# Optimization experiments

Measured on AMD Instinct MI355X. Metric: run time of the kernel, lower is better.

Reference implementation:

```python
import jax, jax.numpy as jnp
import numpy as np

C = 256
GROUPS = 8
EPS = 1e-5


def setup_inputs() -> dict:
    key = jax.random.key(0)
    ks = jax.random.split(key, 7)
    b, c, h, w = 8, C, 64, 64
    x = jax.random.normal(ks[0], (b, c, h, w), dtype=jnp.float32)
    gn_w = jnp.ones((c,), jnp.float32)
    gn_b = jnp.zeros((c,), jnp.float32)
    # 1x1 conv == per-pixel linear; store weights as [out, in]
    qkv_w = jax.random.normal(ks[1], (3 * c, c), dtype=jnp.float32) * (1.0 / np.sqrt(c))
    qkv_b = jnp.zeros((3 * c,), jnp.float32)
    proj_w = jax.random.normal(ks[2], (c, c), dtype=jnp.float32) * (1.0 / np.sqrt(c))
    proj_b = jnp.zeros((c,), jnp.float32)
    return {"x": x, "gn_w": gn_w, "gn_b": gn_b, "qkv_w": qkv_w,
            "qkv_b": qkv_b, "proj_w": proj_w, "proj_b": proj_b}


def _group_norm(x, gamma, beta):
    b, c, h, w = x.shape
    xg = x.reshape(b, GROUPS, c // GROUPS, h * w)
    mean = xg.mean(axis=(2, 3), keepdims=True)
    var = xg.var(axis=(2, 3), keepdims=True)
    xn = ((xg - mean) * jax.lax.rsqrt(var + EPS)).reshape(b, c, h, w)
    return xn * gamma[None, :, None, None] + beta[None, :, None, None]


def reference(x, gn_w, gn_b, qkv_w, qkv_b, proj_w, proj_b):
    b, c, h, w = x.shape
    n = h * w
    xn = _group_norm(x, gn_w, gn_b)
    # 1x1 conv QKV: [b,3c,h,w]
    qkv = jnp.einsum('bchw,oc->bohw', xn, qkv_w) + qkv_b[None, :, None, None]
    q, k, v = jnp.split(qkv, 3, axis=1)
    q = q.reshape(b, c, n)  # [b,c,n]
    k = k.reshape(b, c, n)
    v = v.reshape(b, c, n)
    scale = 1.0 / jnp.sqrt(jnp.asarray(c, x.dtype))
    attn = jax.nn.softmax(jnp.einsum('bcn,bcm->bnm', q, k) * scale, axis=-1)
    out = jnp.einsum('bnm,bcm->bcn', attn, v).reshape(b, c, h, w)
    proj = jnp.einsum('bchw,oc->bohw', out, proj_w) + proj_b[None, :, None, None]
    return x + proj
```

## Files before the change

kernel.cpp:

```cpp
#include <hip/hip_runtime.h>


typedef __bf16 bf16x8 __attribute__((ext_vector_type(8)));
typedef __bf16 bf16x2_t __attribute__((ext_vector_type(2)));
typedef float  f32x16 __attribute__((ext_vector_type(16)));
typedef unsigned short ushort_t;

#define QSCALE 0.09016844005556021f
#define THR_L2 11.541560327111707f

__device__ __forceinline__ unsigned short f2b(float f) {
  return __builtin_bit_cast(unsigned short, (__bf16)f);
}
__device__ __forceinline__ unsigned pk2(float lo, float hi) {
  bf16x2_t p; p[0] = (__bf16)lo; p[1] = (__bf16)hi;
  return __builtin_bit_cast(unsigned, p);
}
__device__ __forceinline__ f32x16 zero16() {
  f32x16 z;
#pragma unroll
  for (int i = 0; i < 16; ++i) z[i] = 0.f;
  return z;
}
__device__ __forceinline__ void gl_lds16(const void* gsrc, void* ldst) {
  __builtin_amdgcn_global_load_lds(
      (const __attribute__((address_space(1))) unsigned int*)gsrc,
      (__attribute__((address_space(3))) unsigned int*)ldst, 16, 0, 0);
}

static const size_t OFF_PART = 0;
static const size_t OFF_WQ   = 4096;
static const size_t OFF_WP   = OFF_WQ + 768*256*2;
static const size_t OFF_XNT  = OFF_WP + 256*256*2;
static const size_t OFF_Q    = OFF_XNT + (size_t)8*4096*256*2;
static const size_t OFF_K    = OFF_Q  + (size_t)8*4096*256*2;
static const size_t OFF_V    = OFF_K  + (size_t)8*4096*256*2;
static const size_t OFF_O    = OFF_XNT;

__global__ __launch_bounds__(256) void k_wconv(const float* wq, const float* wp,
                                               ushort_t* wqb, ushort_t* wpb) {
  int t = blockIdx.x * 256 + threadIdx.x;
  if (t < 24576) {
    int lane = t & 63, k = (t >> 6) & 15, tile = t >> 10;
    const float* src = wq + (size_t)(tile*32 + (lane & 31))*256 + (k*2 + (lane >> 5))*8;
    ushort4 lo, hi;
    lo.x = f2b(src[0]); lo.y = f2b(src[1]); lo.z = f2b(src[2]); lo.w = f2b(src[3]);
    hi.x = f2b(src[4]); hi.y = f2b(src[5]); hi.z = f2b(src[6]); hi.w = f2b(src[7]);
    *(ushort4*)(wqb + (size_t)t*8)     = lo;
    *(ushort4*)(wqb + (size_t)t*8 + 4) = hi;
  }
  if (t < 8192) {
    int lane = t & 63, k = (t >> 6) & 15, tile = t >> 10;
    const float* src = wp + (size_t)(tile*32 + (lane & 31))*256 + (k*2 + (lane >> 5))*8;
    ushort4 lo, hi;
    lo.x = f2b(src[0]); lo.y = f2b(src[1]); lo.z = f2b(src[2]); lo.w = f2b(src[3]);
    hi.x = f2b(src[4]); hi.y = f2b(src[5]); hi.z = f2b(src[6]); hi.w = f2b(src[7]);
    *(ushort4*)(wpb + (size_t)t*8)     = lo;
    *(ushort4*)(wpb + (size_t)t*8 + 4) = hi;
  }
}

__global__ __launch_bounds__(256) void k_stats(const float* x, float* part) {
  int bg = blockIdx.x >> 3, sl = blockIdx.x & 7;
  const float4* p = (const float4*)(x + (size_t)bg*131072u + (size_t)sl*16384u);
  float s = 0.f, ss = 0.f;
  for (int i = threadIdx.x; i < 4096; i += 256) {
    float4 v = p[i];
    s  += (v.x + v.y) + (v.z + v.w);
    ss += (v.x*v.x + v.y*v.y) + (v.z*v.z + v.w*v.w);
  }
#pragma unroll
  for (int m = 1; m < 64; m <<= 1) { s += __shfl_xor(s, m); ss += __shfl_xor(ss, m); }
  __shared__ float ls[4], lq[4];
  int w = threadIdx.x >> 6;
  if ((threadIdx.x & 63) == 0) { ls[w] = s; lq[w] = ss; }
  __syncthreads();
  if (threadIdx.x == 0) {
    part[bg*8 + sl]       = ls[0] + ls[1] + ls[2] + ls[3];
    part[512 + bg*8 + sl] = lq[0] + lq[1] + lq[2] + lq[3];
  }
}

__global__ __launch_bounds__(256) void k_norm_t(const float* x, const float* part,
                                                const float* gw, const float* gb,
                                                ushort_t* xnt) {
  int id = blockIdx.x;
  int b = id & 7, nb = (id >> 3) & 127, cb = id >> 10;
  int bg = b*8 + cb;
  float s = 0.f, q = 0.f;
#pragma unroll
  for (int i = 0; i < 8; ++i) { s += part[bg*8+i]; q += part[512 + bg*8+i]; }
  const float inv_n = 1.f/131072.f;
  float mean = s * inv_n;
  float rstd = rsqrtf(q*inv_n - mean*mean + 1e-5f);

  __shared__ float tile[32][33];
  int tx = threadIdx.x & 31, ty = threadIdx.x >> 5;
  const float* xp = x + ((size_t)b*256 + cb*32)*4096 + nb*32;
#pragma unroll
  for (int r = 0; r < 4; ++r) {
    int cl = ty + r*8;
    int c  = cb*32 + cl;
    float v = xp[(size_t)cl*4096 + tx];
    tile[cl][tx] = (v - mean)*rstd*gw[c] + gb[c];
  }
  __syncthreads();
  int nl = threadIdx.x >> 3, c4 = (threadIdx.x & 7)*4;
  ushort4 o;
  o.x = f2b(tile[c4+0][nl]); o.y = f2b(tile[c4+1][nl]);
  o.z = f2b(tile[c4+2][nl]); o.w = f2b(tile[c4+3][nl]);
  int c0g = cb*32 + c4;
  size_t addr = (size_t)((nb*16 + (c0g >> 4))*64 + nl + 32*((c0g >> 3) & 1))*8 + (c0g & 7);
  *(ushort4*)(xnt + (size_t)b*1048576 + addr) = o;
}

__global__ __launch_bounds__(256, 2) void k_qkv(const ushort_t* xnt, const ushort_t* wqb,
                                                const float* qkvb,
                                                ushort_t* qt, ushort_t* kt, ushort_t* vc) {
  int id = blockIdx.x;
  int b = id & 7, rest = id >> 3;
  int nb = rest & 63, ob = rest >> 6;
  int lane = threadIdx.x & 63, w = threadIdx.x >> 6;
  int ln = lane & 31, h = lane >> 5;
  int o0 = ob*128 + w*32;
  int p0 = nb*64;

  const ushort_t* abase = wqb + (size_t)(ob*4 + w)*8192 + lane*8;
  bf16x8 af[16];
#pragma unroll
  for (int k = 0; k < 16; ++k) af[k] = *(const bf16x8*)(abase + k*512);

  const ushort_t* xb = xnt + (size_t)b*1048576 + (size_t)(nb*2)*8192 + lane*8;
  f32x16 acc0 = zero16(), acc1 = zero16();
#pragma unroll
  for (int k = 0; k < 16; ++k) {
    bf16x8 b0 = *(const bf16x8*)(xb + k*512);
    bf16x8 b1 = *(const bf16x8*)(xb + 8192 + k*512);
    acc0 = __builtin_amdgcn_mfma_f32_32x32x16_bf16(af[k], b0, acc0, 0, 0, 0);
    acc1 = __builtin_amdgcn_mfma_f32_32x32x16_bf16(af[k], b1, acc1, 0, 0, 0);
  }
  int sect = o0 >> 8;
#pragma unroll
  for (int jt = 0; jt < 2; ++jt) {
    f32x16 a = jt ? acc1 : acc0;
    int p = p0 + jt*32 + ln;
#pragma unroll
    for (int rg = 0; rg < 4; ++rg) {
      int ob4 = o0 + rg*8 + h*4;
      float4 bi = *(const float4*)(qkvb + ob4);
      float v0 = a[rg*4+0] + bi.x, v1 = a[rg*4+1] + bi.y;
      float v2 = a[rg*4+2] + bi.z, v3 = a[rg*4+3] + bi.w;
      if (sect == 0) {
        v0 *= QSCALE; v1 *= QSCALE; v2 *= QSCALE; v3 *= QSCALE;
        ushort4 st; st.x = f2b(v0); st.y = f2b(v1); st.z = f2b(v2); st.w = f2b(v3);
        *(ushort4*)(qt + ((size_t)b*4096 + p)*256 + (ob4 & 255)) = st;
      } else if (sect == 1) {
        ushort4 st; st.x = f2b(v0); st.y = f2b(v1); st.z = f2b(v2); st.w = f2b(v3);
        *(ushort4*)(kt + ((size_t)b*4096 + p)*256 + (ob4 & 255)) = st;
      } else {
        int c0 = ob4 - 512;
        vc[((size_t)b*256 + c0+0)*4096 + p] = f2b(v0);
        vc[((size_t)b*256 + c0+1)*4096 + p] = f2b(v1);
        vc[((size_t)b*256 + c0+2)*4096 + p] = f2b(v2);
        vc[((size_t)b*256 + c0+3)*4096 + p] = f2b(v3);
      }
    }
  }
}

__global__ __launch_bounds__(512, 2) void k_attn(const ushort_t* qt, const ushort_t* kt,
                                                 const ushort_t* vc, ushort_t* ot) {
  int id = blockIdx.x;
  int b = id & 7, qb = id >> 3;
  int tid = threadIdx.x;
  int lane = tid & 63, w = tid >> 6;
  int ln = lane & 31, h = lane >> 5;
  int hv = w >> 2;
  int qs = w & 3;
  int q0 = qb*128 + qs*32;

  __shared__ uint4 slds[8192];

  const bf16x8* qrow = (const bf16x8*)(qt + ((size_t)b*4096 + q0 + ln)*256);
  bf16x8 qf[16];
#pragma unroll
  for (int k = 0; k < 16; ++k) qf[k] = qrow[k*2 + h];

  const ushort_t* kb   = kt + (size_t)b*4096*256;
  const ushort_t* vb_g = vc + (size_t)b*256*4096;

  int swz = (lane & 7) ^ ((lane >> 3) & 7);
  const ushort_t* ksrc = kb + (size_t)(w*8 + (lane >> 3))*256 + swz*8;
  const ushort_t* vsrc = vb_g + swz*8;
  int vrow0 = w*32 + (lane >> 3);

  int lnx = ln & 7;
  int koff_base = (hv*4 + (ln >> 3))*256 + lnx*8;

  f32x16 po[8];
#pragma unroll
  for (int t = 0; t < 8; ++t) po[t] = zero16();
  float m_run = -1e30f, l_run = 0.f;

#pragma unroll
  for (int q = 0; q < 4; ++q)
    gl_lds16(ksrc + q*64, &slds[w*256 + q*64]);
#pragma unroll
  for (int q = 0; q < 4; ++q)
    gl_lds16(vsrc + (size_t)(vrow0 + q*8)*4096, &slds[4096 + w*256 + q*64]);

  for (int it = 0; it < 64; ++it) {
    int cur = it & 1, nxt = cur ^ 1;
    __syncthreads();

    if (it < 63) {
      int nmb = (it + 1)*64;
#pragma unroll
      for (int q = 0; q < 4; ++q)
        gl_lds16(ksrc + (size_t)nmb*256 + q*64, &slds[nxt*2048 + w*256 + q*64]);
#pragma unroll
      for (int q = 0; q < 4; ++q)
        gl_lds16(vsrc + (size_t)(vrow0 + q*8)*4096 + nmb,
                 &slds[4096 + nxt*2048 + w*256 + q*64]);
    }

    const uint4* kbase = &slds[cur*2048 + koff_base];
    f32x16 s0 = zero16();
    __builtin_amdgcn_s_setprio(1);
#pragma unroll
    for (int k = 0; k < 16; ++k) {
      int j = k*2 + h;
      bf16x8 kf = *(const bf16x8*)&kbase[(j >> 3)*64 + ((j & 7) ^ lnx)];
      s0 = __builtin_amdgcn_mfma_f32_32x32x16_bf16(kf, qf[k], s0, 0, 0, 0);
    }
    __builtin_amdgcn_s_setprio(0);

    float tmax = s0[0];
#pragma unroll
    for (int r = 1; r < 16; ++r) tmax = fmaxf(tmax, s0[r]);
    tmax = fmaxf(tmax, __shfl_xor(tmax, 32));
    if (__any(tmax > m_run + THR_L2)) {
      float nm    = fmaxf(m_run, tmax);
      float alpha = exp2f(m_run - nm);
      m_run = nm;
      l_run *= alpha;
#pragma unroll
      for (int t = 0; t < 8; ++t)
#pragma unroll
        for (int r = 0; r < 16; ++r) po[t][r] *= alpha;
    }
    float psum = 0.f;
#pragma unroll
    for (int r = 0; r < 16; ++r) {
      s0[r] = exp2f(s0[r] - m_run);
      psum += s0[r];
    }
    psum += __shfl_xor(psum, 32);
    l_run += psum;

    unsigned wpk[8], wsw[8];
#pragma unroll
    for (int k2 = 0; k2 < 8; ++k2) wpk[k2] = pk2(s0[2*k2], s0[2*k2+1]);
#pragma unroll
    for (int k2 = 0; k2 < 8; ++k2) wsw[k2] = __shfl_xor(wpk[k2], 32);
    union { unsigned u[4]; bf16x8 v; } flo, fhi;
    if (h == 0) {
      flo.u[0] = wpk[0]; flo.u[1] = wpk[1]; flo.u[2] = wsw[0]; flo.u[3] = wsw[1];
      fhi.u[0] = wpk[4]; fhi.u[1] = wpk[5]; fhi.u[2] = wsw[4]; fhi.u[3] = wsw[5];
    } else {
      flo.u[0] = wsw[2]; flo.u[1] = wsw[3]; flo.u[2] = wpk[2]; flo.u[3] = wpk[3];
      fhi.u[0] = wsw[6]; fhi.u[1] = wsw[7]; fhi.u[2] = wpk[6]; fhi.u[3] = wpk[7];
    }
    const uint4* vbase = &slds[4096 + cur*2048];
    __builtin_amdgcn_s_setprio(1);
#pragma unroll
    for (int ct = 0; ct < 8; ++ct) {
      int c = ct*32 + ln;
      bf16x8 va  = *(const bf16x8*)&vbase[(c*8 + hv*4 + 0 + h) ^ (c & 7)];
      po[ct] = __builtin_amdgcn_mfma_f32_32x32x16_bf16(va, flo.v, po[ct], 0, 0, 0);
      bf16x8 vb2 = *(const bf16x8*)&vbase[(c*8 + hv*4 + 2 + h) ^ (c & 7)];
      po[ct] = __builtin_amdgcn_mfma_f32_32x32x16_bf16(vb2, fhi.v, po[ct], 0, 0, 0);
    }
    __builtin_amdgcn_s_setprio(0);
  }

  float* fbuf = (float*)slds;
  float* mlb  = fbuf + 8192;
  ushort_t* orow = ot + ((size_t)b*4096 + q0 + ln)*256;

#pragma unroll
  for (int rnd = 0; rnd < 4; ++rnd) {
    __syncthreads();
    if (w == rnd + 4) {
#pragma unroll
      for (int t = 0; t < 8; ++t)
#pragma unroll
        for (int rg = 0; rg < 4; ++rg) {
          float4 d; d.x = po[t][rg*4+0]; d.y = po[t][rg*4+1];
          d.z = po[t][rg*4+2]; d.w = po[t][rg*4+3];
          *(float4*)&fbuf[(t*4+rg)*256 + lane*4] = d;
        }
      mlb[lane] = m_run; mlb[64 + lane] = l_run;
    }
    __syncthreads();
    if (w == rnd) {
      float m2 = mlb[lane], l2 = mlb[64 + lane];
      float m  = fmaxf(m_run, m2);
      float a1 = exp2f(m_run - m), a2 = exp2f(m2 - m);
      float inv = 1.f / (l_run*a1 + l2*a2);
      float f1 = a1*inv, f2 = a2*inv;
#pragma unroll
      for (int ct = 0; ct < 8; ++ct)
#pragma unroll
        for (int rg = 0; rg < 4; ++rg) {
          float4 o2 = *(const float4*)&fbuf[(ct*4+rg)*256 + lane*4];
          ushort4 st;
          st.x = f2b(po[ct][rg*4+0]*f1 + o2.x*f2);
          st.y = f2b(po[ct][rg*4+1]*f1 + o2.y*f2);
          st.z = f2b(po[ct][rg*4+2]*f1 + o2.z*f2);
          st.w = f2b(po[ct][rg*4+3]*f1 + o2.w*f2);
          *(ushort4*)(orow + ct*32 + rg*8 + h*4) = st;
        }
    }
  }
}

__global__ __launch_bounds__(256, 2) void k_proj(const ushort_t* ot, const ushort_t* wpb,
                                                 const float* pjb, const float* x, float* y) {
  int id = blockIdx.x;
  int b = id & 7, rest = id >> 3;
  int pb = rest & 31, nb = rest >> 5;
  int lane = threadIdx.x & 63, w = threadIdx.x >> 6;
  int ln = lane & 31, h = lane >> 5;
  int p0 = pb*128 + w*32;

  const bf16x8* arow = (const bf16x8*)(ot + ((size_t)b*4096 + p0 + ln)*256);
  bf16x8 af[16];
#pragma unroll
  for (int k = 0; k < 16; ++k) af[k] = arow[k*2 + h];

  const ushort_t* wb = wpb + (size_t)(nb*2)*8192 + lane*8;
  f32x16 acc0 = zero16(), acc1 = zero16();
#pragma unroll
  for (int k = 0; k < 16; ++k) {
    bf16x8 w0 = *(const bf16x8*)(wb + k*512);
    bf16x8 w1 = *(const bf16x8*)(wb + 8192 + k*512);
    acc0 = __builtin_amdgcn_mfma_f32_32x32x16_bf16(af[k], w0, acc0, 0, 0, 0);
    acc1 = __builtin_amdgcn_mfma_f32_32x32x16_bf16(af[k], w1, acc1, 0, 0, 0);
  }
#pragma unroll
  for (int jt = 0; jt < 2; ++jt) {
    f32x16 a = jt ? acc1 : acc0;
    int o = nb*64 + jt*32 + ln;
    float bias = pjb[o];
    const float* xr = x + ((size_t)b*256 + o)*4096;
    float* yr = y + ((size_t)b*256 + o)*4096;
#pragma unroll
    for (int rg = 0; rg < 4; ++rg) {
      int pbase = p0 + rg*8 + h*4;
      float4 xv = *(const float4*)(xr + pbase);
      float4 ov;
      ov.x = xv.x + a[rg*4+0] + bias;
      ov.y = xv.y + a[rg*4+1] + bias;
      ov.z = xv.z + a[rg*4+2] + bias;
      ov.w = xv.w + a[rg*4+3] + bias;
      *(float4*)(yr + pbase) = ov;
    }
  }
}

extern "C" void kernel_launch(void* const* d_in, const int* in_sizes, int n_in,
                              void* d_out, int out_size, void* d_ws, size_t ws_size,
                              hipStream_t stream) {
  const float* x  = (const float*)d_in[0];
  const float* gw = (const float*)d_in[1];
  const float* gb = (const float*)d_in[2];
  const float* qw = (const float*)d_in[3];
  const float* qb = (const float*)d_in[4];
  const float* pw = (const float*)d_in[5];
  const float* pb = (const float*)d_in[6];

  char* ws = (char*)d_ws;
  float*    part = (float*)(ws + OFF_PART);
  ushort_t* wqb  = (ushort_t*)(ws + OFF_WQ);
  ushort_t* wpb  = (ushort_t*)(ws + OFF_WP);
  ushort_t* xnt  = (ushort_t*)(ws + OFF_XNT);
  ushort_t* qt   = (ushort_t*)(ws + OFF_Q);
  ushort_t* kt   = (ushort_t*)(ws + OFF_K);
  ushort_t* vc   = (ushort_t*)(ws + OFF_V);
  ushort_t* ot   = (ushort_t*)(ws + OFF_O);
  float* y = (float*)d_out;

  k_wconv <<<96,   256, 0, stream>>>(qw, pw, wqb, wpb);
  k_stats <<<512,  256, 0, stream>>>(x, part);
  k_norm_t<<<8192, 256, 0, stream>>>(x, part, gw, gb, xnt);
  k_qkv   <<<3072, 256, 0, stream>>>(xnt, wqb, qb, qt, kt, vc);
  k_attn  <<<256,  512, 0, stream>>>(qt, kt, vc, ot);
  k_proj  <<<1024, 256, 0, stream>>>(ot, wpb, pb, x, y);
}
```

Baseline: 235.3 us.

## Shrink attention blocks to 4 waves and split K/V loads within iteration

The attention kernel moves from 512-thread blocks covering 128 queries to 256-thread blocks covering 64 queries, doubling the grid and halving LDS to a single K and a single V buffer. The double-buffered prefetch is replaced by a staggered schedule: V for the current tile loads while QK^T runs, and the next K tile loads after a mid-iteration barrier while softmax and PV run. The aim is to cut LDS footprint, allowing more blocks per CU, and to overlap loads with compute without double buffering. The cost is twice the K/V global traffic per query (smaller query tiles), an extra barrier per iteration, and less prefetch lead time.

```diff
diff --git a/kernel.cpp b/kernel.cpp
--- a/kernel.cpp
+++ b/kernel.cpp
@@ -168,18 +168,18 @@
   }
 }
 
-__global__ __launch_bounds__(512, 2) void k_attn(const ushort_t* qt, const ushort_t* kt,
+__global__ __launch_bounds__(256, 2) void k_attn(const ushort_t* qt, const ushort_t* kt,
                                                  const ushort_t* vc, ushort_t* ot) {
   int id = blockIdx.x;
   int b = id & 7, qb = id >> 3;
   int tid = threadIdx.x;
   int lane = tid & 63, w = tid >> 6;
   int ln = lane & 31, h = lane >> 5;
-  int hv = w >> 2;
-  int qs = w & 3;
-  int q0 = qb*128 + qs*32;
-
-  __shared__ uint4 slds[8192];
+  int hv = w >> 1;
+  int qs = w & 1;
+  int q0 = qb*64 + qs*32;
+
+  __shared__ uint4 slds[4096];
 
   const bf16x8* qrow = (const bf16x8*)(qt + ((size_t)b*4096 + q0 + ln)*256);
   bf16x8 qf[16];
@@ -189,10 +189,13 @@
   const ushort_t* kb   = kt + (size_t)b*4096*256;
   const ushort_t* vb_g = vc + (size_t)b*256*4096;
 
-  int swz = (lane & 7) ^ ((lane >> 3) & 7);
-  const ushort_t* ksrc = kb + (size_t)(w*8 + (lane >> 3))*256 + swz*8;
-  const ushort_t* vsrc = vb_g + swz*8;
-  int vrow0 = w*32 + (lane >> 3);
+  int rl = (tid >> 3) & 7;
+  int cg = tid >> 6;
+  int cl = (tid & 7) ^ rl;
+  const ushort_t* ksrc = kb + (size_t)rl*256 + (cg*8 + cl)*8;
+  uint4* kdst = &slds[tid];
+  const ushort_t* vsrcB = vb_g + (size_t)(tid >> 3)*4096 + cl*8;
+  uint4* vdst = &slds[2048 + tid];
 
   int lnx = ln & 7;
   int koff_base = (hv*4 + (ln >> 3))*256 + lnx*8;
@@ -203,28 +206,18 @@
   float m_run = -1e30f, l_run = 0.f;
 
 #pragma unroll
-  for (int q = 0; q < 4; ++q)
-    gl_lds16(ksrc + q*64, &slds[w*256 + q*64]);
-#pragma unroll
-  for (int q = 0; q < 4; ++q)
-    gl_lds16(vsrc + (size_t)(vrow0 + q*8)*4096, &slds[4096 + w*256 + q*64]);
+  for (int q = 0; q < 8; ++q)
+    gl_lds16(ksrc + (size_t)(q*8)*256, kdst + q*256);
 
   for (int it = 0; it < 64; ++it) {
-    int cur = it & 1, nxt = cur ^ 1;
+    int mb = it*64;
     __syncthreads();
 
-    if (it < 63) {
-      int nmb = (it + 1)*64;
-#pragma unroll
-      for (int q = 0; q < 4; ++q)
-        gl_lds16(ksrc + (size_t)nmb*256 + q*64, &slds[nxt*2048 + w*256 + q*64]);
-#pragma unroll
-      for (int q = 0; q < 4; ++q)
-        gl_lds16(vsrc + (size_t)(vrow0 + q*8)*4096 + nmb,
-                 &slds[4096 + nxt*2048 + w*256 + q*64]);
-    }
-
-    const uint4* kbase = &slds[cur*2048 + koff_base];
+#pragma unroll
+    for (int q = 0; q < 8; ++q)
+      gl_lds16(vsrcB + (size_t)(q*32)*4096 + mb, vdst + q*256);
+
+    const uint4* kbase = &slds[koff_base];
     f32x16 s0 = zero16();
     __builtin_amdgcn_s_setprio(1);
 #pragma unroll
@@ -234,6 +227,14 @@
       s0 = __builtin_amdgcn_mfma_f32_32x32x16_bf16(kf, qf[k], s0, 0, 0, 0);
     }
     __builtin_amdgcn_s_setprio(0);
+
+    __syncthreads();
+
+    if (it < 63) {
+#pragma unroll
+      for (int q = 0; q < 8; ++q)
+        gl_lds16(ksrc + (size_t)(mb + 64 + q*8)*256, kdst + q*256);
+    }
 
     float tmax = s0[0];
 #pragma unroll
@@ -271,7 +272,7 @@
       flo.u[0] = wsw[2]; flo.u[1] = wsw[3]; flo.u[2] = wpk[2]; flo.u[3] = wpk[3];
       fhi.u[0] = wsw[6]; fhi.u[1] = wsw[7]; fhi.u[2] = wpk[6]; fhi.u[3] = wpk[7];
     }
-    const uint4* vbase = &slds[4096 + cur*2048];
+    const uint4* vbase = &slds[2048];
     __builtin_amdgcn_s_setprio(1);
 #pragma unroll
     for (int ct = 0; ct < 8; ++ct) {
@@ -285,13 +286,13 @@
   }
 
   float* fbuf = (float*)slds;
-  float* mlb  = fbuf + 8192;
+  float* mlb  = (float*)&slds[2048];
   ushort_t* orow = ot + ((size_t)b*4096 + q0 + ln)*256;
 
 #pragma unroll
-  for (int rnd = 0; rnd < 4; ++rnd) {
+  for (int rnd = 0; rnd < 2; ++rnd) {
     __syncthreads();
-    if (w == rnd + 4) {
+    if (w == rnd + 2) {
 #pragma unroll
       for (int t = 0; t < 8; ++t)
 #pragma unroll
@@ -395,6 +396,6 @@
   k_stats <<<512,  256, 0, stream>>>(x, part);
   k_norm_t<<<8192, 256, 0, stream>>>(x, part, gw, gb, xnt);
   k_qkv   <<<3072, 256, 0, stream>>>(xnt, wqb, qb, qt, kt, vc);
-  k_attn  <<<256,  512, 0, stream>>>(qt, kt, vc, ot);
+  k_attn  <<<512,  256, 0, stream>>>(qt, kt, vc, ot);
   k_proj  <<<1024, 256, 0, stream>>>(ot, wpb, pb, x, y);
 }
```

After: 257.6 us. 9.5% more time.

## Software-pipeline attention loop: overlap next QK^T MFMA with current softmax and PV

Applied to the files above, without the earlier changes.

Restructures the flash-attention inner loop so the QK^T scores for tile it are computed while softmax and the PV MFMAs run on tile it-1, with a prologue and epilogue for the first and last tiles. K and V loads are staggered: K is prefetched one tile ahead, and V for the current tile is loaded while the previous tile's V is consumed. The aim is to hide the serial latency of exp and softmax behind MFMA work. In exchange it keeps an extra 16-register score accumulator live, which raises register pressure and may reduce occupancy, and it changes the LDS buffer reuse ordering.

```diff
diff --git a/kernel.cpp b/kernel.cpp
--- a/kernel.cpp
+++ b/kernel.cpp
@@ -201,6 +201,7 @@
 #pragma unroll
   for (int t = 0; t < 8; ++t) po[t] = zero16();
   float m_run = -1e30f, l_run = 0.f;
+  f32x16 s_prev;
 
 #pragma unroll
   for (int q = 0; q < 4; ++q)
@@ -209,35 +210,52 @@
   for (int q = 0; q < 4; ++q)
     gl_lds16(vsrc + (size_t)(vrow0 + q*8)*4096, &slds[4096 + w*256 + q*64]);
 
-  for (int it = 0; it < 64; ++it) {
-    int cur = it & 1, nxt = cur ^ 1;
-    __syncthreads();
-
-    if (it < 63) {
-      int nmb = (it + 1)*64;
-#pragma unroll
-      for (int q = 0; q < 4; ++q)
-        gl_lds16(ksrc + (size_t)nmb*256 + q*64, &slds[nxt*2048 + w*256 + q*64]);
-#pragma unroll
-      for (int q = 0; q < 4; ++q)
-        gl_lds16(vsrc + (size_t)(vrow0 + q*8)*4096 + nmb,
-                 &slds[4096 + nxt*2048 + w*256 + q*64]);
-    }
-
-    const uint4* kbase = &slds[cur*2048 + koff_base];
-    f32x16 s0 = zero16();
+  __syncthreads();
+  {
+#pragma unroll
+    for (int q = 0; q < 4; ++q)
+      gl_lds16(ksrc + (size_t)64*256 + q*64, &slds[2048 + w*256 + q*64]);
+    const uint4* kbase = &slds[koff_base];
+    f32x16 sc = zero16();
     __builtin_amdgcn_s_setprio(1);
 #pragma unroll
     for (int k = 0; k < 16; ++k) {
       int j = k*2 + h;
       bf16x8 kf = *(const bf16x8*)&kbase[(j >> 3)*64 + ((j & 7) ^ lnx)];
-      s0 = __builtin_amdgcn_mfma_f32_32x32x16_bf16(kf, qf[k], s0, 0, 0, 0);
+      sc = __builtin_amdgcn_mfma_f32_32x32x16_bf16(kf, qf[k], sc, 0, 0, 0);
     }
     __builtin_amdgcn_s_setprio(0);
-
-    float tmax = s0[0];
-#pragma unroll
-    for (int r = 1; r < 16; ++r) tmax = fmaxf(tmax, s0[r]);
+    s_prev = sc;
+  }
+
+  for (int it = 1; it < 64; ++it) {
+    int cur = it & 1, prv = cur ^ 1;
+    __syncthreads();
+
+    if (it < 63) {
+      int nmb = (it + 1)*64;
+#pragma unroll
+      for (int q = 0; q < 4; ++q)
+        gl_lds16(ksrc + (size_t)nmb*256 + q*64, &slds[prv*2048 + w*256 + q*64]);
+    }
+#pragma unroll
+    for (int q = 0; q < 4; ++q)
+      gl_lds16(vsrc + (size_t)(vrow0 + q*8)*4096 + it*64,
+               &slds[4096 + cur*2048 + w*256 + q*64]);
+
+    __builtin_amdgcn_s_setprio(1);
+    const uint4* kbase = &slds[cur*2048 + koff_base];
+    f32x16 s_cur = zero16();
+#pragma unroll
+    for (int k = 0; k < 16; ++k) {
+      int j = k*2 + h;
+      bf16x8 kf = *(const bf16x8*)&kbase[(j >> 3)*64 + ((j & 7) ^ lnx)];
+      s_cur = __builtin_amdgcn_mfma_f32_32x32x16_bf16(kf, qf[k], s_cur, 0, 0, 0);
+    }
+
+    float tmax = s_prev[0];
+#pragma unroll
+    for (int r = 1; r < 16; ++r) tmax = fmaxf(tmax, s_prev[r]);
     tmax = fmaxf(tmax, __shfl_xor(tmax, 32));
     if (__any(tmax > m_run + THR_L2)) {
       float nm    = fmaxf(m_run, tmax);
@@ -252,15 +270,15 @@
     float psum = 0.f;
 #pragma unroll
     for (int r = 0; r < 16; ++r) {
-      s0[r] = exp2f(s0[r] - m_run);
-      psum += s0[r];
+      s_prev[r] = exp2f(s_prev[r] - m_run);
+      psum += s_prev[r];
     }
     psum += __shfl_xor(psum, 32);
     l_run += psum;
 
     unsigned wpk[8], wsw[8];
 #pragma unroll
-    for (int k2 = 0; k2 < 8; ++k2) wpk[k2] = pk2(s0[2*k2], s0[2*k2+1]);
+    for (int k2 = 0; k2 < 8; ++k2) wpk[k2] = pk2(s_prev[2*k2], s_prev[2*k2+1]);
 #pragma unroll
     for (int k2 = 0; k2 < 8; ++k2) wsw[k2] = __shfl_xor(wpk[k2], 32);
     union { unsigned u[4]; bf16x8 v; } flo, fhi;
@@ -271,7 +289,60 @@
       flo.u[0] = wsw[2]; flo.u[1] = wsw[3]; flo.u[2] = wpk[2]; flo.u[3] = wpk[3];
       fhi.u[0] = wsw[6]; fhi.u[1] = wsw[7]; fhi.u[2] = wpk[6]; fhi.u[3] = wpk[7];
     }
-    const uint4* vbase = &slds[4096 + cur*2048];
+
+    const uint4* vbase = &slds[4096 + prv*2048];
+#pragma unroll
+    for (int ct = 0; ct < 8; ++ct) {
+      int c = ct*32 + ln;
+      bf16x8 va  = *(const bf16x8*)&vbase[(c*8 + hv*4 + 0 + h) ^ (c & 7)];
+      po[ct] = __builtin_amdgcn_mfma_f32_32x32x16_bf16(va, flo.v, po[ct], 0, 0, 0);
+      bf16x8 vb2 = *(const bf16x8*)&vbase[(c*8 + hv*4 + 2 + h) ^ (c & 7)];
+      po[ct] = __builtin_amdgcn_mfma_f32_32x32x16_bf16(vb2, fhi.v, po[ct], 0, 0, 0);
+    }
+    __builtin_amdgcn_s_setprio(0);
+
+    s_prev = s_cur;
+  }
+
+  __syncthreads();
+  {
+    float tmax = s_prev[0];
+#pragma unroll
+    for (int r = 1; r < 16; ++r) tmax = fmaxf(tmax, s_prev[r]);
+    tmax = fmaxf(tmax, __shfl_xor(tmax, 32));
+    if (__any(tmax > m_run + THR_L2)) {
+      float nm    = fmaxf(m_run, tmax);
+      float alpha = exp2f(m_run - nm);
+      m_run = nm;
+      l_run *= alpha;
+#pragma unroll
+      for (int t = 0; t < 8; ++t)
+#pragma unroll
+        for (int r = 0; r < 16; ++r) po[t][r] *= alpha;
+    }
+    float psum = 0.f;
+#pragma unroll
+    for (int r = 0; r < 16; ++r) {
+      s_prev[r] = exp2f(s_prev[r] - m_run);
+      psum += s_prev[r];
+    }
+    psum += __shfl_xor(psum, 32);
+    l_run += psum;
+
+    unsigned wpk[8], wsw[8];
+#pragma unroll
+    for (int k2 = 0; k2 < 8; ++k2) wpk[k2] = pk2(s_prev[2*k2], s_prev[2*k2+1]);
+#pragma unroll
+    for (int k2 = 0; k2 < 8; ++k2) wsw[k2] = __shfl_xor(wpk[k2], 32);
+    union { unsigned u[4]; bf16x8 v; } flo, fhi;
+    if (h == 0) {
+      flo.u[0] = wpk[0]; flo.u[1] = wpk[1]; flo.u[2] = wsw[0]; flo.u[3] = wsw[1];
+      fhi.u[0] = wpk[4]; fhi.u[1] = wpk[5]; fhi.u[2] = wsw[4]; fhi.u[3] = wsw[5];
+    } else {
+      flo.u[0] = wsw[2]; flo.u[1] = wsw[3]; flo.u[2] = wpk[2]; flo.u[3] = wpk[3];
+      fhi.u[0] = wsw[6]; fhi.u[1] = wsw[7]; fhi.u[2] = wpk[6]; fhi.u[3] = wpk[7];
+    }
+    const uint4* vbase = &slds[4096 + 2048];
     __builtin_amdgcn_s_setprio(1);
 #pragma unroll
     for (int ct = 0; ct < 8; ++ct) {
```

New measurement: 290.1 us. 1.23x slower.
